# Optimization experiments

Measured on AMD Instinct MI355X. Metric: run time of the kernel, lower is better.

The kernel has to match this reference:

```python
import jax, jax.numpy as jnp
from jax import lax
import numpy as np

B, T, D_IN, H = 64, 256, 512, 1024


def setup_inputs() -> dict:
    key = jax.random.key(0)
    k_x, k_ih, k_hh = jax.random.split(key, 3)
    x = jax.random.normal(k_x, (B, T, D_IN), dtype=jnp.float32)
    # Xavier-uniform-like scaling for weights; biases start at zero (init_weights).
    lim_ih = (6.0 / (4 * H + D_IN)) ** 0.5
    lim_hh = (6.0 / (4 * H + H)) ** 0.5
    w_ih = jax.random.uniform(k_ih, (4 * H, D_IN), jnp.float32, -lim_ih, lim_ih)
    w_hh = jax.random.uniform(k_hh, (4 * H, H), jnp.float32, -lim_hh, lim_hh)
    b_ih = jnp.zeros((4 * H,), jnp.float32)
    b_hh = jnp.zeros((4 * H,), jnp.float32)
    return {"x": x, "w_ih": w_ih, "w_hh": w_hh, "b_ih": b_ih, "b_hh": b_hh}


def reference(x, w_ih, w_hh, b_ih, b_hh):
    # x: [B, T, D_in]; gate order is (i, f, g, o) per the chunk in the source.
    bsz = x.shape[0]
    hid = w_hh.shape[1]
    # Precompute input projection for all timesteps: [B, T, 4H]
    x_proj = jnp.einsum('btd,gd->btg', x, w_ih) + b_ih + b_hh

    def step(carry, xp_t):
        h, c = carry
        gates = xp_t + h @ w_hh.T  # [B, 4H]
        i_g, f_g, g_g, o_g = jnp.split(gates, 4, axis=-1)
        i_t = jax.nn.sigmoid(i_g)
        f_t = jax.nn.sigmoid(f_g)
        g_t = jnp.tanh(g_g)
        o_t = jax.nn.sigmoid(o_g)
        c_new = f_t * c + i_t * g_t
        h_new = o_t * jnp.tanh(c_new)
        return (h_new, c_new), h_new

    h0 = jnp.zeros((bsz, hid), x.dtype)
    c0 = jnp.zeros((bsz, hid), x.dtype)
    (_, _), h_seq = lax.scan(step, (h0, c0), jnp.swapaxes(x_proj, 0, 1))  # [T, B, H]
    return jnp.swapaxes(h_seq, 0, 1)  # [B, T, H]
```

## Files before the change

kernel.cpp:

```cpp
#include <hip/hip_runtime.h>
#include <math.h>

#define BB   64
#define TT   256
#define DIN  512
#define HH   1024
#define KF   1536
#define NG   4096

typedef short  bf16x8 __attribute__((ext_vector_type(8)));
typedef float  f32x4  __attribute__((ext_vector_type(4)));

#define WF_OFF 0
#define XB_OFF (12582912)
#define HB_OFF (XB_OFF + 16777216)
#define CT_OFF (HB_OFF + 131072)

__device__ __forceinline__ float sig_(float x) { return 1.f / (1.f + expf(-x)); }
__device__ __forceinline__ float th_(float x)  { return tanhf(x); }

__device__ __forceinline__ unsigned short f2b(float f) {
    union { float f; unsigned u; } v; v.f = f;
    unsigned r = (v.u + 0x7FFF + ((v.u >> 16) & 1)) >> 16;
    return (unsigned short)r;
}

__global__ __launch_bounds__(256) void conv_w(
    const float* __restrict__ wih, const float* __restrict__ whh,
    unsigned short* __restrict__ Wf)
{
    int gid = blockIdx.x * 256 + threadIdx.x;
    int n   = gid / 192;
    int kg  = gid - n * 192;
    const float* src = (kg < 64) ? (wih + (size_t)n * DIN + kg * 8)
                                 : (whh + (size_t)n * HH + (kg - 64) * 8);
    float4 a = *(const float4*)(src);
    float4 b = *(const float4*)(src + 4);
    unsigned short o[8] = { f2b(a.x), f2b(a.y), f2b(a.z), f2b(a.w),
                            f2b(b.x), f2b(b.y), f2b(b.z), f2b(b.w) };
    *(uint4*)(Wf + (size_t)n * KF + kg * 8) = *(const uint4*)o;
}

__global__ __launch_bounds__(256) void conv_x(
    const float* __restrict__ x, unsigned short* __restrict__ xb)
{
    int gid = blockIdx.x * 256 + threadIdx.x;
    int t   = gid >> 12;
    int rem = gid & 4095;
    int b   = rem >> 6;
    int kg  = rem & 63;
    const float* src = x + (size_t)b * (TT * DIN) + (size_t)t * DIN + kg * 8;
    float4 a = *(const float4*)(src);
    float4 c = *(const float4*)(src + 4);
    unsigned short o[8] = { f2b(a.x), f2b(a.y), f2b(a.z), f2b(a.w),
                            f2b(c.x), f2b(c.y), f2b(c.z), f2b(c.w) };
    *(uint4*)(xb + (size_t)t * (BB * DIN) + (size_t)b * DIN + kg * 8) = *(const uint4*)o;
}

__global__ __launch_bounds__(256) void lstm_step(
    const unsigned short* __restrict__ Wf, const unsigned short* __restrict__ xb,
    unsigned short* __restrict__ hb, float* __restrict__ cT,
    const float* __restrict__ bih, const float* __restrict__ bhh,
    float* __restrict__ out, int t)
{
    __shared__ float scr[4][16][17];

    const int tid  = threadIdx.x;
    const int lane = tid & 63;
    const int wv   = tid >> 6;
    const int lo   = lane & 15;
    const int hi   = lane >> 4;

    const int gq = lo >> 2;
    const int jo = lo & 3;
    const int j0 = blockIdx.x * 4;
    const int n  = gq * HH + j0 + jo;
    const unsigned short* wrow = Wf + (size_t)n * KF;

    const int b = 16 * wv + lo;

    const float bias = bih[n] + bhh[n];
    f32x4 acc = { bias, bias, bias, bias };

    const unsigned short* xrow = xb + (size_t)t * (BB * DIN) + (size_t)b * DIN;
#pragma unroll
    for (int kk = 0; kk < 16; ++kk) {
        const int k = kk * 32 + hi * 8;
        bf16x8 af = *(const bf16x8*)(xrow + k);
        bf16x8 bf = *(const bf16x8*)(wrow + k);
        acc = __builtin_amdgcn_mfma_f32_16x16x32_bf16(af, bf, acc, 0, 0, 0);
    }

    if (t > 0) {
#pragma unroll
        for (int kk = 0; kk < 32; ++kk) {
            const int jb = kk * 8 + hi * 2;
            const unsigned short* hp = hb + (size_t)jb * 256 + b * 4;
            uint2 v0 = *(const uint2*)(hp);
            uint2 v1 = *(const uint2*)(hp + 256);
            union { uint4 u; bf16x8 f; } uu;
            uu.u.x = v0.x; uu.u.y = v0.y; uu.u.z = v1.x; uu.u.w = v1.y;
            bf16x8 bf = *(const bf16x8*)(wrow + 512 + kk * 32 + hi * 8);
            acc = __builtin_amdgcn_mfma_f32_16x16x32_bf16(uu.f, bf, acc, 0, 0, 0);
        }
    }

#pragma unroll
    for (int r = 0; r < 4; ++r)
        scr[wv][4 * hi + r][lo] = acc[r];
    __syncthreads();

    const int bidx = 16 * wv + lo;
    const int jj   = j0 + hi;
    float vi = scr[wv][lo][ 0 + hi];
    float vf = scr[wv][lo][ 4 + hi];
    float vg = scr[wv][lo][ 8 + hi];
    float vo = scr[wv][lo][12 + hi];

    float i_t = sig_(vi);
    float f_t = sig_(vf);
    float g_t = th_(vg);
    float o_t = sig_(vo);
    float cprev = (t > 0) ? cT[jj * 64 + bidx] : 0.f;
    float cn = fmaf(f_t, cprev, i_t * g_t);
    cT[jj * 64 + bidx] = cn;
    float hn = o_t * th_(cn);

    out[(size_t)bidx * (TT * HH) + (size_t)t * HH + jj] = hn;
    hb[(size_t)blockIdx.x * 256 + bidx * 4 + hi] = f2b(hn);
}

extern "C" void kernel_launch(void* const* d_in, const int* in_sizes, int n_in,
                              void* d_out, int out_size, void* d_ws, size_t ws_size,
                              hipStream_t stream)
{
    const float* x   = (const float*)d_in[0];
    const float* wih = (const float*)d_in[1];
    const float* whh = (const float*)d_in[2];
    const float* bih = (const float*)d_in[3];
    const float* bhh = (const float*)d_in[4];
    float* out = (float*)d_out;

    char* ws = (char*)d_ws;
    unsigned short* Wf = (unsigned short*)(ws + WF_OFF);
    unsigned short* xb = (unsigned short*)(ws + XB_OFF);
    unsigned short* hb = (unsigned short*)(ws + HB_OFF);
    float*          cT = (float*)(ws + CT_OFF);

    conv_w<<<dim3(3072), dim3(256), 0, stream>>>(wih, whh, Wf);
    conv_x<<<dim3(4096), dim3(256), 0, stream>>>(x, xb);

    for (int t = 0; t < TT; ++t) {
        lstm_step<<<dim3(256), dim3(256), 0, stream>>>(Wf, xb, hb, cT, bih, bhh, out, t);
    }
}
```

Before: 3.294 ms.

## Fuse all LSTM timesteps into one persistent kernel with grid barrier

Replaces the 256 per-timestep launches with a single persistent kernel. Each block converts its weight rows to bf16 once and keeps them in registers, holds the cell state in a register, and double-buffers h in global memory with an atomic-counter grid barrier between steps. Two accumulators split the MFMA dependency chain, and the input-projection MFMAs are issued before the barrier wait so they overlap it. This removes per-step launch overhead and the repeated weight reloads, but relies on all 256 blocks being co-resident and holds 48 bf16x8 weight vectors in registers per thread, which could spill.

```diff
diff --git a/kernel.cpp b/kernel.cpp
--- a/kernel.cpp
+++ b/kernel.cpp
@@ -5,40 +5,27 @@
 #define TT   256
 #define DIN  512
 #define HH   1024
-#define KF   1536
-#define NG   4096
+#define NBLK 256
 
 typedef short  bf16x8 __attribute__((ext_vector_type(8)));
 typedef float  f32x4  __attribute__((ext_vector_type(4)));
 
-#define WF_OFF 0
-#define XB_OFF (12582912)
-#define HB_OFF (XB_OFF + 16777216)
-#define CT_OFF (HB_OFF + 131072)
+#define XB_OFF  0
+#define HB_OFF  16777216
+#define BAR_OFF (16777216 + 262144)
 
 __device__ __forceinline__ float sig_(float x) { return 1.f / (1.f + expf(-x)); }
-__device__ __forceinline__ float th_(float x)  { return tanhf(x); }
 
 __device__ __forceinline__ unsigned short f2b(float f) {
     union { float f; unsigned u; } v; v.f = f;
-    unsigned r = (v.u + 0x7FFF + ((v.u >> 16) & 1)) >> 16;
-    return (unsigned short)r;
+    return (unsigned short)((v.u + 0x7FFF + ((v.u >> 16) & 1)) >> 16);
 }
 
-__global__ __launch_bounds__(256) void conv_w(
-    const float* __restrict__ wih, const float* __restrict__ whh,
-    unsigned short* __restrict__ Wf)
-{
-    int gid = blockIdx.x * 256 + threadIdx.x;
-    int n   = gid / 192;
-    int kg  = gid - n * 192;
-    const float* src = (kg < 64) ? (wih + (size_t)n * DIN + kg * 8)
-                                 : (whh + (size_t)n * HH + (kg - 64) * 8);
-    float4 a = *(const float4*)(src);
-    float4 b = *(const float4*)(src + 4);
-    unsigned short o[8] = { f2b(a.x), f2b(a.y), f2b(a.z), f2b(a.w),
-                            f2b(b.x), f2b(b.y), f2b(b.z), f2b(b.w) };
-    *(uint4*)(Wf + (size_t)n * KF + kg * 8) = *(const uint4*)o;
+__device__ __forceinline__ bf16x8 pack8(const float* p) {
+    union { unsigned short s[8]; bf16x8 v; } u;
+#pragma unroll
+    for (int e = 0; e < 8; ++e) u.s[e] = f2b(p[e]);
+    return u.v;
 }
 
 __global__ __launch_bounds__(256) void conv_x(
@@ -50,18 +37,22 @@
     int b   = rem >> 6;
     int kg  = rem & 63;
     const float* src = x + (size_t)b * (TT * DIN) + (size_t)t * DIN + kg * 8;
-    float4 a = *(const float4*)(src);
-    float4 c = *(const float4*)(src + 4);
-    unsigned short o[8] = { f2b(a.x), f2b(a.y), f2b(a.z), f2b(a.w),
-                            f2b(c.x), f2b(c.y), f2b(c.z), f2b(c.w) };
+    float tmp[8];
+    *(float4*)(tmp)     = *(const float4*)(src);
+    *(float4*)(tmp + 4) = *(const float4*)(src + 4);
+    unsigned short o[8];
+#pragma unroll
+    for (int e = 0; e < 8; ++e) o[e] = f2b(tmp[e]);
     *(uint4*)(xb + (size_t)t * (BB * DIN) + (size_t)b * DIN + kg * 8) = *(const uint4*)o;
 }
 
-__global__ __launch_bounds__(256) void lstm_step(
-    const unsigned short* __restrict__ Wf, const unsigned short* __restrict__ xb,
-    unsigned short* __restrict__ hb, float* __restrict__ cT,
+__global__ void init_bar(unsigned* bar) { if (threadIdx.x == 0) *bar = 0u; }
+
+__global__ __launch_bounds__(256, 1) void lstm_all(
+    const float* __restrict__ wih, const float* __restrict__ whh,
     const float* __restrict__ bih, const float* __restrict__ bhh,
-    float* __restrict__ out, int t)
+    const unsigned short* __restrict__ xb, unsigned short* __restrict__ hb,
+    unsigned* bar, float* __restrict__ out)
 {
     __shared__ float scr[4][16][17];
 
@@ -75,59 +66,91 @@
     const int jo = lo & 3;
     const int j0 = blockIdx.x * 4;
     const int n  = gq * HH + j0 + jo;
-    const unsigned short* wrow = Wf + (size_t)n * KF;
 
-    const int b = 16 * wv + lo;
+    const int b    = 16 * wv + lo;
+    const int bidx = 16 * wv + lo;
+    const int jj   = j0 + hi;
 
-    const float bias = bih[n] + bhh[n];
-    f32x4 acc = { bias, bias, bias, bias };
-
-    const unsigned short* xrow = xb + (size_t)t * (BB * DIN) + (size_t)b * DIN;
+    const float* wihrow = wih + (size_t)n * DIN;
+    const float* whhrow = whh + (size_t)n * HH;
+    bf16x8 wx[16], wh[32];
 #pragma unroll
     for (int kk = 0; kk < 16; ++kk) {
         const int k = kk * 32 + hi * 8;
-        bf16x8 af = *(const bf16x8*)(xrow + k);
-        bf16x8 bf = *(const bf16x8*)(wrow + k);
-        acc = __builtin_amdgcn_mfma_f32_16x16x32_bf16(af, bf, acc, 0, 0, 0);
+        float tmp[8];
+        *(float4*)(tmp)     = *(const float4*)(wihrow + k);
+        *(float4*)(tmp + 4) = *(const float4*)(wihrow + k + 4);
+        wx[kk] = pack8(tmp);
     }
+#pragma unroll
+    for (int kk = 0; kk < 32; ++kk) {
+        const int k = kk * 32 + hi * 8;
+        float tmp[8];
+        *(float4*)(tmp)     = *(const float4*)(whhrow + k);
+        *(float4*)(tmp + 4) = *(const float4*)(whhrow + k + 4);
+        wh[kk] = pack8(tmp);
+    }
+    const float bias = bih[n] + bhh[n];
+    float creg = 0.f;
 
-    if (t > 0) {
+    for (int t = 0; t < TT; ++t) {
+        f32x4 accA = { bias, bias, bias, bias };
+        f32x4 accB = { 0.f, 0.f, 0.f, 0.f };
+
+        const unsigned short* xrow = xb + (size_t)t * (BB * DIN) + (size_t)b * DIN;
 #pragma unroll
-        for (int kk = 0; kk < 32; ++kk) {
-            const int jb = kk * 8 + hi * 2;
-            const unsigned short* hp = hb + (size_t)jb * 256 + b * 4;
-            uint2 v0 = *(const uint2*)(hp);
-            uint2 v1 = *(const uint2*)(hp + 256);
-            union { uint4 u; bf16x8 f; } uu;
-            uu.u.x = v0.x; uu.u.y = v0.y; uu.u.z = v1.x; uu.u.w = v1.y;
-            bf16x8 bf = *(const bf16x8*)(wrow + 512 + kk * 32 + hi * 8);
-            acc = __builtin_amdgcn_mfma_f32_16x16x32_bf16(uu.f, bf, acc, 0, 0, 0);
+        for (int kk = 0; kk < 16; kk += 2) {
+            bf16x8 a0 = *(const bf16x8*)(xrow + kk * 32 + hi * 8);
+            bf16x8 a1 = *(const bf16x8*)(xrow + (kk + 1) * 32 + hi * 8);
+            accA = __builtin_amdgcn_mfma_f32_16x16x32_bf16(a0, wx[kk],     accA, 0, 0, 0);
+            accB = __builtin_amdgcn_mfma_f32_16x16x32_bf16(a1, wx[kk + 1], accB, 0, 0, 0);
         }
-    }
+
+        if (t > 0) {
+            if (tid == 0) {
+                const unsigned target = (unsigned)t * NBLK;
+                while (__hip_atomic_load(bar, __ATOMIC_RELAXED, __HIP_MEMORY_SCOPE_AGENT) < target)
+                    __builtin_amdgcn_s_sleep(4);
+                (void)__hip_atomic_load(bar, __ATOMIC_ACQUIRE, __HIP_MEMORY_SCOPE_AGENT);
+            }
+            __syncthreads();
+
+            const unsigned short* hrow = hb + (size_t)((t - 1) & 1) * (BB * HH) + (size_t)b * HH;
+#pragma unroll
+            for (int kk = 0; kk < 32; kk += 2) {
+                bf16x8 a0 = *(const bf16x8*)(hrow + kk * 32 + hi * 8);
+                bf16x8 a1 = *(const bf16x8*)(hrow + (kk + 1) * 32 + hi * 8);
+                accA = __builtin_amdgcn_mfma_f32_16x16x32_bf16(a0, wh[kk],     accA, 0, 0, 0);
+                accB = __builtin_amdgcn_mfma_f32_16x16x32_bf16(a1, wh[kk + 1], accB, 0, 0, 0);
+            }
+        }
+        f32x4 acc = accA + accB;
 
 #pragma unroll
-    for (int r = 0; r < 4; ++r)
-        scr[wv][4 * hi + r][lo] = acc[r];
-    __syncthreads();
+        for (int r = 0; r < 4; ++r)
+            scr[wv][4 * hi + r][lo] = acc[r];
+        __syncthreads();
 
-    const int bidx = 16 * wv + lo;
-    const int jj   = j0 + hi;
-    float vi = scr[wv][lo][ 0 + hi];
-    float vf = scr[wv][lo][ 4 + hi];
-    float vg = scr[wv][lo][ 8 + hi];
-    float vo = scr[wv][lo][12 + hi];
+        float vi = scr[wv][lo][ 0 + hi];
+        float vf = scr[wv][lo][ 4 + hi];
+        float vg = scr[wv][lo][ 8 + hi];
+        float vo = scr[wv][lo][12 + hi];
 
-    float i_t = sig_(vi);
-    float f_t = sig_(vf);
-    float g_t = th_(vg);
-    float o_t = sig_(vo);
-    float cprev = (t > 0) ? cT[jj * 64 + bidx] : 0.f;
-    float cn = fmaf(f_t, cprev, i_t * g_t);
-    cT[jj * 64 + bidx] = cn;
-    float hn = o_t * th_(cn);
+        float i_t = sig_(vi);
+        float f_t = sig_(vf);
+        float g_t = tanhf(vg);
+        float o_t = sig_(vo);
+        float cn  = fmaf(f_t, creg, i_t * g_t);
+        creg = cn;
+        float hn = o_t * tanhf(cn);
 
-    out[(size_t)bidx * (TT * HH) + (size_t)t * HH + jj] = hn;
-    hb[(size_t)blockIdx.x * 256 + bidx * 4 + hi] = f2b(hn);
+        out[(size_t)bidx * (TT * HH) + (size_t)t * HH + jj] = hn;
+        hb[(size_t)(t & 1) * (BB * HH) + (size_t)bidx * HH + jj] = f2b(hn);
+
+        __syncthreads();
+        if (tid == 0)
+            __hip_atomic_fetch_add(bar, 1u, __ATOMIC_RELEASE, __HIP_MEMORY_SCOPE_AGENT);
+    }
 }
 
 extern "C" void kernel_launch(void* const* d_in, const int* in_sizes, int n_in,
@@ -142,15 +165,11 @@
     float* out = (float*)d_out;
 
     char* ws = (char*)d_ws;
-    unsigned short* Wf = (unsigned short*)(ws + WF_OFF);
     unsigned short* xb = (unsigned short*)(ws + XB_OFF);
     unsigned short* hb = (unsigned short*)(ws + HB_OFF);
-    float*          cT = (float*)(ws + CT_OFF);
+    unsigned*       bar = (unsigned*)(ws + BAR_OFF);
 
-    conv_w<<<dim3(3072), dim3(256), 0, stream>>>(wih, whh, Wf);
     conv_x<<<dim3(4096), dim3(256), 0, stream>>>(x, xb);
-
-    for (int t = 0; t < TT; ++t) {
-        lstm_step<<<dim3(256), dim3(256), 0, stream>>>(Wf, xb, hb, cT, bih, bhh, out, t);
-    }
+    init_bar<<<dim3(1), dim3(64), 0, stream>>>(bar);
+    lstm_all<<<dim3(256), dim3(256), 0, stream>>>(wih, whh, bih, bhh, xb, hb, bar, out);
 }
```

New measurement: 3.843 ms. +16.7%, slower.
